# Kernel optimization log

Hardware: AMD Instinct MI355X
Metric: run time of the kernel (lower is better)

The kernel has to match this reference:

```python
import jax, jax.numpy as jnp
from jax import lax
import numpy as np

T = 8   # num_samples
D = 7   # num_nodes
K = 3   # topk


def _normalize(v):
    return v / jnp.maximum(jnp.linalg.norm(v, axis=-1, keepdims=True), 1e-12)


def _pool(x):
    # AdaptiveMaxPool2d(1): [B,H,N,C,h,w] -> [B,H,N,C]
    return x.max(axis=(-2, -1))


def _sepconv(x, dw, dwb, pw, pwb):
    # depthwise 3x3 (pad 1) + pointwise 1x1, NCHW
    c = x.shape[1]
    y = lax.conv_general_dilated(x, dw, (1, 1), ((1, 1), (1, 1)),
                                 dimension_numbers=('NCHW', 'OIHW', 'NCHW'),
                                 feature_group_count=c)
    y = y + dwb[None, :, None, None]
    y = lax.conv_general_dilated(y, pw, (1, 1), 'VALID',
                                 dimension_numbers=('NCHW', 'OIHW', 'NCHW'))
    return y + pwb[None, :, None, None]


def _conv_iter(x, A, dw, dwb, pw, pwb):
    # x: [B,H,N,C,h,w], A: [B,H,M,N] -> aggregate then sepconv update
    x = jnp.einsum('bhnm,bhmcij->bhncij', A, x)
    B, H, N, C, h, w = x.shape
    y = x.transpose(0, 2, 1, 3, 4, 5).reshape(B * N, H * C, h, w)
    y = _sepconv(y, dw, dwb, pw, pwb)
    return y.reshape(B, N, H, C, h, w).transpose(0, 2, 1, 3, 4, 5)


def reference(x, alpha_if, alpha_tm1, alpha_rev, alpha_tm2,
              bias_if, bias_tm1, bias_rev, bias_tm2,
              if_dw, if_dwb, if_pw, if_pwb,
              tm1_dw, tm1_dwb, tm1_pw, tm1_pwb,
              rev_dw, rev_dwb, rev_pw, rev_pwb,
              tm2_dw, tm2_dwb, tm2_pw, tm2_pwb,
              tr_dw, tr_dwb, tr_pw, tr_pwb):
    B, H, Nall, C, hh, ww = x.shape
    normal = x[:, :, 1:]            # [B,H,T*D,C,h,w]
    master = x[:, :, 0:1]           # [B,H,1,C,h,w]
    # 'b h (t d) c i j -> (b t) h d c i j'
    normal = normal.reshape(B, H, T, D, C, hh, ww).transpose(0, 2, 1, 3, 4, 5, 6).reshape(B * T, H, D, C, hh, ww)

    # inter-frame adjacency
    vn = _normalize(_pool(normal))
    A = jax.nn.softmax(jnp.einsum('bhnc,bhmc->bhnm', vn, vn) / alpha_if + bias_if, axis=-1)
    normal = _conv_iter(normal, A, if_dw, if_dwb, if_pw, if_pwb)

    # to master 1
    temp = normal.reshape(B, T, H, D, C, hh, ww).transpose(0, 2, 1, 3, 4, 5, 6).reshape(B, H, T * D, C, hh, ww)
    all_node = jnp.concatenate([master, temp], axis=2)   # [B,H,57,...]
    vn = _normalize(_pool(all_node))
    A = jax.nn.softmax(jnp.einsum('bhnc,bhmc->bhnm', vn[:, :, 0:1], vn) / alpha_tm1 + bias_tm1, axis=-1)
    master = _conv_iter(all_node, A, tm1_dw, tm1_dwb, tm1_pw, tm1_pwb)  # [B,H,1,C,h,w]

    # transform normal nodes
    Bt = B * T
    y = normal.transpose(0, 2, 1, 3, 4, 5).reshape(Bt * D, H * C, hh, ww)
    y = _sepconv(y, tr_dw, tr_dwb, tr_pw, tr_pwb)
    normal = y.reshape(Bt, D, H, C, hh, ww).transpose(0, 2, 1, 3, 4, 5)

    # reverse: topk MOST-DISSIMILAR frames (largest=False on similarity)
    temp = normal.reshape(B, T, H, D, C, hh, ww).transpose(0, 2, 1, 3, 4, 5, 6)  # [B,H,T,D,C,h,w]
    main = temp[:, :, :, -1]                                 # [B,H,T,C,h,w]
    mv = _normalize(_pool(main))                              # [B,H,T,C]
    Asim = jnp.einsum('bhtc,bhsc->bhts', mv, mv)
    idx = lax.top_k(-Asim, K)[1]                              # [B,H,T,K] smallest-sim frames
    bi = jnp.arange(B)[:, None, None, None]
    hi = jnp.arange(H)[None, :, None, None]
    sel = temp[bi, hi, idx]                                   # [B,H,T,K,D,C,h,w]
    different = sel.transpose(0, 2, 1, 3, 4, 5, 6, 7).reshape(Bt, H, K * D, C, hh, ww)

    vd = _normalize(_pool(different))
    vo = _normalize(_pool(normal))
    A = jax.nn.softmax(-jnp.einsum('bhnc,bhmc->bhnm', vo, vd) / alpha_rev + bias_rev, axis=-1)
    normal = _conv_iter(different, A, rev_dw, rev_dwb, rev_pw, rev_pwb) + normal

    # to master 2
    temp = normal.reshape(B, T, H, D, C, hh, ww).transpose(0, 2, 1, 3, 4, 5, 6).reshape(B, H, T * D, C, hh, ww)
    all_node = jnp.concatenate([master, temp], axis=2)
    vn = _normalize(_pool(all_node))
    A = jax.nn.softmax(jnp.einsum('bhnc,bhmc->bhnm', vn[:, :, 0:1], vn) / alpha_tm2 + bias_tm2, axis=-1)
    master = _conv_iter(all_node, A, tm2_dw, tm2_dwb, tm2_pw, tm2_pwb)
    return master[:, :, 0]                                    # [B,H,C,h,w]


def setup_inputs() -> dict:
    key = jax.random.key(0)
    ks = jax.random.split(key, 16)
    B, H, C, hh, ww = 4, 4, 128, 14, 14
    DIM = 512
    w_scale = 0.05

    def sep(k):
        k1, k2 = jax.random.split(k)
        return (jax.random.normal(k1, (DIM, 1, 3, 3), jnp.float32) * w_scale,
                jnp.zeros((DIM,), jnp.float32),
                jax.random.normal(k2, (DIM, DIM, 1, 1), jnp.float32) * w_scale,
                jnp.zeros((DIM,), jnp.float32))

    if_dw, if_dwb, if_pw, if_pwb = sep(ks[1])
    tm1_dw, tm1_dwb, tm1_pw, tm1_pwb = sep(ks[2])
    rev_dw, rev_dwb, rev_pw, rev_pwb = sep(ks[3])
    tm2_dw, tm2_dwb, tm2_pw, tm2_pwb = sep(ks[4])
    tr_dw, tr_dwb, tr_pw, tr_pwb = sep(ks[5])

    return dict(
        x=jax.random.normal(ks[0], (B, H, 1 + T * D, C, hh, ww), jnp.float32),
        alpha_if=jnp.ones((), jnp.float32), alpha_tm1=jnp.ones((), jnp.float32),
        alpha_rev=jnp.ones((), jnp.float32), alpha_tm2=jnp.ones((), jnp.float32),
        bias_if=jnp.zeros((D, D), jnp.float32),
        bias_tm1=jnp.zeros((1, 1 + T * D), jnp.float32),
        bias_rev=jnp.zeros((D, K * D), jnp.float32),
        bias_tm2=jnp.zeros((1, 1 + T * D), jnp.float32),
        if_dw=if_dw, if_dwb=if_dwb, if_pw=if_pw, if_pwb=if_pwb,
        tm1_dw=tm1_dw, tm1_dwb=tm1_dwb, tm1_pw=tm1_pw, tm1_pwb=tm1_pwb,
        rev_dw=rev_dw, rev_dwb=rev_dwb, rev_pw=rev_pw, rev_pwb=rev_pwb,
        tm2_dw=tm2_dw, tm2_dwb=tm2_dwb, tm2_pw=tm2_pw, tm2_pwb=tm2_pwb,
        tr_dw=tr_dw, tr_dwb=tr_dwb, tr_pw=tr_pw, tr_pwb=tr_pwb,
    )
```

## Files before the change

kernel.cpp:

```cpp
#include <hip/hip_runtime.h>
#include <hip/hip_bf16.h>
#include <float.h>
#include <math.h>

#define B_    4
#define H_    4
#define T_    8
#define D_    7
#define C_    128
#define HH_   14
#define S_    196
#define BT_   32
#define HC_   512
#define NODE_ 57
#define K_    3
#define KD_   21

#define BIG_  (BT_*D_*HC_*S_)
#define MS_   (B_*HC_*S_)
#define UB_   (BT_*D_*S_)
#define UM_   (B_*S_)
#define NT_   24
#define WS_   1024

typedef unsigned short u16;
typedef unsigned int   u32;
typedef short bf16x8 __attribute__((ext_vector_type(8)));
typedef float f32x4  __attribute__((ext_vector_type(4)));

__device__ __forceinline__ float wave_max(float v){
    #pragma unroll
    for(int o=32;o>0;o>>=1) v = fmaxf(v, __shfl_xor(v,o,64));
    return v;
}
__device__ __forceinline__ float wave_sum(float v){
    #pragma unroll
    for(int o=32;o>0;o>>=1) v += __shfl_xor(v,o,64);
    return v;
}
__device__ __forceinline__ u16 f2bf(float f){
    u32 u = __float_as_uint(f);
    u += 0x7FFF + ((u>>16)&1);
    return (u16)(u>>16);
}
__device__ __forceinline__ float bf2f(u16 h){ return __uint_as_float(((u32)h)<<16); }

__device__ __forceinline__ void gld16(const void* g, void* l){
    __builtin_amdgcn_global_load_lds(
        (__attribute__((address_space(1))) void*)(void*)g,
        (__attribute__((address_space(3))) void*)l, 16, 0, 0);
}

__global__ void k_pool_x(const float* __restrict__ x, float* __restrict__ out){
    int v = blockIdx.x*4 + (threadIdx.x>>6);
    int lane = threadIdx.x & 63;
    int c = v & (C_-1);
    int r = v >> 7;
    int d = r % D_; r /= D_;
    int h = r & (H_-1); r >>= 2;
    int bt = r;
    int b = bt >> 3, t = bt & 7;
    const float* row = x + ((size_t)((b*H_+h)*NODE_ + 1 + t*D_ + d)*C_ + c)*S_;
    float m = -FLT_MAX;
    for(int s=lane; s<S_; s+=64) m = fmaxf(m, row[s]);
    m = wave_max(m);
    if(lane==0) out[v] = m;
}

__global__ void k_pool_conv(const float* __restrict__ in, float* __restrict__ out){
    int v = blockIdx.x*4 + (threadIdx.x>>6);
    int lane = threadIdx.x & 63;
    int c = v & (C_-1);
    int r = v >> 7;
    int d = r % D_; r /= D_;
    int h = r & (H_-1); r >>= 2;
    int bt = r;
    const float* row = in + ((size_t)((bt*D_+d)*HC_ + h*C_ + c))*S_;
    float m = -FLT_MAX;
    for(int s=lane; s<S_; s+=64) m = fmaxf(m, row[s]);
    m = wave_max(m);
    if(lane==0) out[v] = m;
}

__global__ void k_pool_x_master(const float* __restrict__ x, float* __restrict__ out){
    int v = blockIdx.x*4 + (threadIdx.x>>6);
    int lane = threadIdx.x & 63;
    int c = v & (C_-1);
    int h = (v>>7) & (H_-1);
    int b = v >> 9;
    const float* row = x + ((size_t)((b*H_+h)*NODE_)*C_ + c)*S_;
    float m = -FLT_MAX;
    for(int s=lane; s<S_; s+=64) m = fmaxf(m, row[s]);
    m = wave_max(m);
    if(lane==0) out[v] = m;
}

__global__ void k_pool_m1(const float* __restrict__ in, float* __restrict__ out){
    int v = blockIdx.x*4 + (threadIdx.x>>6);
    int lane = threadIdx.x & 63;
    int c = v & (C_-1);
    int h = (v>>7) & (H_-1);
    int b = v >> 9;
    const float* row = in + ((size_t)(b*HC_ + h*C_ + c))*S_;
    float m = -FLT_MAX;
    for(int s=lane; s<S_; s+=64) m = fmaxf(m, row[s]);
    m = wave_max(m);
    if(lane==0) out[v] = m;
}

__global__ void k_normalize(float* __restrict__ v){
    int vec = blockIdx.x;
    float val = v[(size_t)vec*C_ + threadIdx.x];
    float ss = wave_sum(val*val);
    __shared__ float sh[2];
    if((threadIdx.x&63)==0) sh[threadIdx.x>>6] = ss;
    __syncthreads();
    float tot = sh[0]+sh[1];
    v[(size_t)vec*C_ + threadIdx.x] = val / fmaxf(sqrtf(tot), 1e-12f);
}

__global__ void k_A_if(const float* __restrict__ vn, const float* __restrict__ bias,
                       const float* __restrict__ alpha_p, float* __restrict__ A){
    int bh = blockIdx.x;
    __shared__ float vs[D_*C_];
    __shared__ float z[D_][D_];
    for(int e=threadIdx.x; e<D_*C_; e+=64) vs[e] = vn[(size_t)bh*D_*C_ + e];
    __syncthreads();
    float alpha = alpha_p[0];
    if(threadIdx.x < D_*D_){
        int n = threadIdx.x/D_, m = threadIdx.x%D_;
        float acc=0.f;
        for(int c=0;c<C_;c++) acc += vs[n*C_+c]*vs[m*C_+c];
        z[n][m] = acc/alpha + bias[n*D_+m];
    }
    __syncthreads();
    if(threadIdx.x < D_){
        int n = threadIdx.x;
        float mx=-FLT_MAX;
        for(int m=0;m<D_;m++) mx=fmaxf(mx,z[n][m]);
        float e[D_]; float sum=0.f;
        for(int m=0;m<D_;m++){ e[m]=expf(z[n][m]-mx); sum+=e[m]; }
        for(int m=0;m<D_;m++) A[((size_t)bh*D_+n)*D_+m] = e[m]/sum;
    }
}

__global__ void k_A_tm(const float* __restrict__ vm, const float* __restrict__ vnrm,
                       const float* __restrict__ bias, const float* __restrict__ alpha_p,
                       float* __restrict__ A){
    int bh = blockIdx.x;
    int b = bh>>2, h = bh&3;
    __shared__ float v0[C_];
    __shared__ float z[NODE_];
    for(int e=threadIdx.x;e<C_;e+=64) v0[e]=vm[(size_t)bh*C_+e];
    __syncthreads();
    float alpha=alpha_p[0];
    if(threadIdx.x<NODE_){
        int m=threadIdx.x;
        float acc=0.f;
        if(m==0){
            for(int c=0;c<C_;c++) acc+=v0[c]*v0[c];
        } else {
            int t=(m-1)/D_, d=(m-1)%D_;
            const float* vp = vnrm + (size_t)(((b*T_+t)*H_+h)*D_+d)*C_;
            for(int c=0;c<C_;c++) acc+=v0[c]*vp[c];
        }
        z[m]=acc/alpha + bias[m];
    }
    __syncthreads();
    if(threadIdx.x==0){
        float mx=-FLT_MAX;
        for(int m=0;m<NODE_;m++) mx=fmaxf(mx,z[m]);
        float sum=0.f;
        for(int m=0;m<NODE_;m++){ z[m]=expf(z[m]-mx); sum+=z[m]; }
        for(int m=0;m<NODE_;m++) A[(size_t)bh*NODE_+m]=z[m]/sum;
    }
}

__global__ void k_topk(const float* __restrict__ voHat, int* __restrict__ idx){
    int bh = blockIdx.x;
    int b = bh>>2, h = bh&3;
    __shared__ float mv[T_][C_];
    __shared__ float As[T_][T_];
    for(int e=threadIdx.x;e<T_*C_;e+=64){
        int t=e>>7, c=e&(C_-1);
        mv[t][c]=voHat[(size_t)(((b*T_+t)*H_+h)*D_+(D_-1))*C_+c];
    }
    __syncthreads();
    {
        int t=threadIdx.x>>3, s2=threadIdx.x&7;
        float acc=0.f;
        for(int c=0;c<C_;c++) acc+=mv[t][c]*mv[s2][c];
        As[t][s2]=acc;
    }
    __syncthreads();
    if(threadIdx.x<T_){
        int t=threadIdx.x;
        bool used[T_];
        for(int j=0;j<T_;j++) used[j]=false;
        for(int k=0;k<K_;k++){
            float mn=FLT_MAX; int bi=0;
            for(int s2=0;s2<T_;s2++){
                if(!used[s2] && As[t][s2]<mn){ mn=As[t][s2]; bi=s2; }
            }
            used[bi]=true;
            idx[((size_t)bh*T_+t)*K_+k]=bi;
        }
    }
}

__global__ void k_A_rev(const float* __restrict__ voHat, const int* __restrict__ idx,
                        const float* __restrict__ bias, const float* __restrict__ alpha_p,
                        float* __restrict__ A){
    int bth = blockIdx.x;
    int bt = bth>>2, h = bth&3;
    int b = bt>>3, t = bt&7;
    __shared__ float vo[D_][C_];
    __shared__ float vd[KD_][C_];
    __shared__ float z[D_][KD_];
    for(int e=threadIdx.x;e<D_*C_;e+=256){
        int n=e>>7, c=e&(C_-1);
        vo[n][c]=voHat[(size_t)((bt*H_+h)*D_+n)*C_+c];
    }
    for(int e=threadIdx.x;e<KD_*C_;e+=256){
        int m=e>>7, c=e&(C_-1);
        int k=m/D_, dp=m%D_;
        int tt=idx[((size_t)(b*H_+h)*T_+t)*K_+k];
        vd[m][c]=voHat[(size_t)(((b*T_+tt)*H_+h)*D_+dp)*C_+c];
    }
    __syncthreads();
    float alpha=alpha_p[0];
    if(threadIdx.x<D_*KD_){
        int n=threadIdx.x/KD_, m=threadIdx.x%KD_;
        float acc=0.f;
        for(int c=0;c<C_;c++) acc+=vo[n][c]*vd[m][c];
        z[n][m] = -acc/alpha + bias[n*KD_+m];
    }
    __syncthreads();
    if(threadIdx.x<D_){
        int n=threadIdx.x;
        float mx=-FLT_MAX;
        for(int m=0;m<KD_;m++) mx=fmaxf(mx,z[n][m]);
        float sum=0.f;
        for(int m=0;m<KD_;m++){ z[n][m]=expf(z[n][m]-mx); sum+=z[n][m]; }
        for(int m=0;m<KD_;m++) A[(size_t)((bt*H_+h)*D_+n)*KD_+m]=z[n][m]/sum;
    }
}

__launch_bounds__(256)
__global__ void k_agg_if(const float* __restrict__ x, const float* __restrict__ A,
                         float* __restrict__ out){
    int bt = blockIdx.x / 392;
    int p  = (blockIdx.x % 392)*256 + threadIdx.x;
    int b = bt>>3, t = bt&7;
    __shared__ float Ash[4][49];
    if(threadIdx.x < 196) Ash[threadIdx.x/49][threadIdx.x%49] = A[(size_t)bt*196 + threadIdx.x];
    __syncthreads();
    int hc = p / S_;
    int s  = p - hc*S_;
    int h = hc>>7, c = hc&127;
    const float* xp = x + ((size_t)((b*H_+h)*NODE_ + 1 + t*D_)*C_ + c)*S_ + s;
    float acc[D_];
    #pragma unroll
    for(int d=0;d<D_;d++) acc[d]=0.f;
    #pragma unroll
    for(int m=0;m<D_;m++){
        float xv = xp[(size_t)m*C_*S_];
        #pragma unroll
        for(int d=0;d<D_;d++) acc[d] += Ash[h][d*7+m]*xv;
    }
    size_t ob = ((size_t)bt*D_*HC_ + hc)*S_ + s;
    #pragma unroll
    for(int d=0;d<D_;d++) out[ob + (size_t)d*HC_*S_] = acc[d];
}

__launch_bounds__(256)
__global__ void k_agg_rev(const float* __restrict__ n2, const float* __restrict__ A,
                          const int* __restrict__ idx, float* __restrict__ out){
    int blk = blockIdx.x;
    int q  = blk % 98;
    int h  = (blk/98) & 3;
    int bt = blk / 392;
    int b = bt>>3, t = bt&7;
    int p  = q*256 + threadIdx.x;
    int c = p / S_;
    int s = p - c*S_;
    __shared__ float Ash[147];
    __shared__ int tts[3];
    if(threadIdx.x<147) Ash[threadIdx.x] = A[(size_t)(bt*4+h)*147 + threadIdx.x];
    if(threadIdx.x>=160 && threadIdx.x<163)
        tts[threadIdx.x-160] = idx[(size_t)((b*4+h)*8+t)*3 + (threadIdx.x-160)];
    __syncthreads();
    float acc[D_];
    #pragma unroll
    for(int d=0;d<D_;d++) acc[d]=0.f;
    #pragma unroll
    for(int k=0;k<K_;k++){
        int tt = tts[k];
        const float* np = n2 + ((size_t)((b*T_+tt)*D_)*HC_ + h*C_ + c)*S_ + s;
        #pragma unroll
        for(int dp=0;dp<D_;dp++){
            float xv = np[(size_t)dp*HC_*S_];
            #pragma unroll
            for(int d=0;d<D_;d++) acc[d] += Ash[d*21 + k*7 + dp]*xv;
        }
    }
    size_t ob = ((size_t)bt*D_*HC_ + h*C_ + c)*S_ + s;
    #pragma unroll
    for(int d=0;d<D_;d++) out[ob + (size_t)d*HC_*S_] = acc[d];
}

__global__ void k_agg_tm(const float* __restrict__ mastersrc, int master_is_x,
                         const float* __restrict__ normal, const float* __restrict__ A,
                         float* __restrict__ out){
    int i = blockIdx.x*256 + threadIdx.x;
    int s = i % S_;
    int r = i / S_;
    int hc = r & (HC_-1);
    int b = r >> 9;
    int h = hc >> 7, c = hc & (C_-1);
    const float* Ap = A + (size_t)(b*H_+h)*NODE_;
    float m0;
    if(master_is_x) m0 = mastersrc[((size_t)((b*H_+h)*NODE_)*C_ + c)*S_ + s];
    else            m0 = mastersrc[(size_t)(b*HC_+hc)*S_ + s];
    float acc = Ap[0]*m0;
    for(int t=0;t<T_;t++){
        const float* np = normal + ((size_t)((b*T_+t)*D_)*HC_+hc)*S_+s;
        #pragma unroll
        for(int d=0;d<D_;d++)
            acc += Ap[1+t*D_+d]*np[(size_t)d*HC_*S_];
    }
    out[i]=acc;
}

__launch_bounds__(256)
__global__ void k_dwsplit(const float* __restrict__ in, const float* __restrict__ w,
                          const float* __restrict__ bias,
                          u16* __restrict__ Xh, u16* __restrict__ Xl){
    int img = blockIdx.x >> 5;
    int ch0 = (blockIdx.x & 31) * 16;
    __shared__ float ti[16][S_];
    __shared__ float to[16][S_];
    int tid = threadIdx.x;
    for(int e=tid; e<16*S_; e+=256){
        int chl = e/S_, s = e%S_;
        ti[chl][s] = in[((size_t)img*HC_ + ch0 + chl)*S_ + s];
    }
    __syncthreads();
    for(int e=tid; e<16*S_; e+=256){
        int chl = e/S_, s = e%S_;
        int ch = ch0 + chl;
        int y = s/HH_, xx = s%HH_;
        float acc = bias[ch];
        #pragma unroll
        for(int ky=0;ky<3;ky++){
            int yy=y+ky-1;
            if(yy<0||yy>=HH_) continue;
            #pragma unroll
            for(int kx=0;kx<3;kx++){
                int xx2=xx+kx-1;
                if(xx2<0||xx2>=HH_) continue;
                acc += ti[chl][yy*HH_+xx2]*w[ch*9+ky*3+kx];
            }
        }
        to[chl][s]=acc;
    }
    __syncthreads();
    for(int e=tid; e<16*S_; e+=256){
        int s = e>>4, chl = e&15;
        float f = to[chl][s];
        u16 h = f2bf(f);
        float lo = f - bf2f(h);
        size_t o = ((size_t)img*S_ + s)*HC_ + ch0 + chl;
        Xh[o] = h;
        Xl[o] = f2bf(lo);
    }
}

__global__ void k_prepW(const float* __restrict__ Wg, u16* __restrict__ Waug){
    int i = blockIdx.x*256 + threadIdx.x;
    int oc = i >> 9, ic = i & 511;
    float f = Wg[i];
    u16 h = f2bf(f);
    float lo = f - bf2f(h);
    size_t base = (size_t)oc*WS_;
    Waug[base + ic]       = h;
    Waug[base + 512 + ic] = f2bf(lo);
}

__launch_bounds__(512)
__global__ void k_pwmfma(const u16* __restrict__ Xh, const u16* __restrict__ Xl,
                         const u16* __restrict__ Waug, const float* __restrict__ bias,
                         const float* __restrict__ res, float* __restrict__ out,
                         int nwg, int utot){
    __shared__ u16 SM[2][16384];
    const int tid  = threadIdx.x;
    const int q = nwg >> 3, r = nwg & 7;
    int xcd = blockIdx.x & 7, j = blockIdx.x >> 3;
    int L = xcd*q + (xcd < r ? xcd : r) + j;
    const int u0   = (L >> 2) * 128;
    const int oc0  = (L & 3) * 128;
    const int lane = tid & 63;
    const int w    = tid >> 6;
    const int wr   = w >> 1, wc = w & 1;
    const int l15  = lane & 15, lg = lane >> 4;

    f32x4 acc[2][4];
    #pragma unroll
    for(int mi=0;mi<2;mi++)
        #pragma unroll
        for(int ni=0;ni<4;ni++)
            acc[mi][ni] = (f32x4){0.f,0.f,0.f,0.f};

    auto STAGE = [&](int t){
        int jj, wk, xk; const u16* Xp;
        if(t < 16){ jj = t>>1; wk = (t&1) ? 512 + jj*64 : jj*64; Xp = Xh; xk = jj*64; }
        else      { jj = t-16; wk = jj*64;                        Xp = Xl; xk = jj*64; }
        u16* Asb = SM[t&1];
        u16* Bsb = Asb + 8192;
        #pragma unroll
        for(int i=0;i<2;i++){
            int seg = w*2 + i;
            int row = seg*8 + (lane>>3);
            int cg  = (lane&7) ^ (lane>>3);
            gld16(Waug + (size_t)(oc0+row)*WS_ + wk + cg*8, Asb + seg*512);
            gld16(Xp   + (size_t)(u0 +row)*512 + xk + cg*8, Bsb + seg*512);
        }
    };
    auto COMPUTE = [&](int cur){
        const u16* Asb = SM[cur];
        const u16* Bsb = SM[cur] + 8192;
        #pragma unroll
        for(int ks=0;ks<2;ks++){
            bf16x8 a[2], b[4];
            #pragma unroll
            for(int mi=0;mi<2;mi++){
                int row = wr*32 + mi*16 + l15;
                int ch  = ((ks<<2) + lg) ^ (row & 7);
                a[mi] = *(const bf16x8*)(Asb + row*64 + ch*8);
            }
            #pragma unroll
            for(int ni=0;ni<4;ni++){
                int row = wc*64 + ni*16 + l15;
                int ch  = ((ks<<2) + lg) ^ (row & 7);
                b[ni] = *(const bf16x8*)(Bsb + row*64 + ch*8);
            }
            #pragma unroll
            for(int mi=0;mi<2;mi++)
                #pragma unroll
                for(int ni=0;ni<4;ni++)
                    acc[mi][ni] = __builtin_amdgcn_mfma_f32_16x16x32_bf16(a[mi], b[ni], acc[mi][ni], 0,0,0);
        }
    };

    STAGE(0);
    for(int t=0; t<NT_; t++){
        if(t+1 < NT_){
            STAGE(t+1);
            asm volatile("s_waitcnt vmcnt(4)" ::: "memory");
        } else {
            asm volatile("s_waitcnt vmcnt(0)" ::: "memory");
        }
        __builtin_amdgcn_s_barrier();
        asm volatile("" ::: "memory");
        COMPUTE(t&1);
        asm volatile("" ::: "memory");
        __builtin_amdgcn_s_barrier();
    }

    #pragma unroll
    for(int ni=0;ni<4;ni++){
        int u = u0 + wc*64 + ni*16 + l15;
        if(u >= utot) continue;
        int img = u / S_, s = u - img*S_;
        #pragma unroll
        for(int mi=0;mi<2;mi++){
            int ocb = oc0 + wr*32 + mi*16 + lg*4;
            #pragma unroll
            for(int q2=0;q2<4;q2++){
                int oc = ocb + q2;
                size_t oidx = ((size_t)img*HC_ + oc)*S_ + s;
                float v = acc[mi][ni][q2] + bias[oc];
                if(res) v += res[oidx];
                out[oidx] = v;
            }
        }
    }
}

extern "C" void kernel_launch(void* const* d_in, const int* in_sizes, int n_in,
                              void* d_out, int out_size, void* d_ws, size_t ws_size,
                              hipStream_t stream){
    (void)in_sizes; (void)n_in; (void)out_size; (void)ws_size;
    const float* x         = (const float*)d_in[0];
    const float* alpha_if  = (const float*)d_in[1];
    const float* alpha_tm1 = (const float*)d_in[2];
    const float* alpha_rev = (const float*)d_in[3];
    const float* alpha_tm2 = (const float*)d_in[4];
    const float* bias_if   = (const float*)d_in[5];
    const float* bias_tm1  = (const float*)d_in[6];
    const float* bias_rev  = (const float*)d_in[7];
    const float* bias_tm2  = (const float*)d_in[8];
    const float* if_dw =(const float*)d_in[9];  const float* if_dwb =(const float*)d_in[10];
    const float* if_pw =(const float*)d_in[11]; const float* if_pwb =(const float*)d_in[12];
    const float* tm1_dw=(const float*)d_in[13]; const float* tm1_dwb=(const float*)d_in[14];
    const float* tm1_pw=(const float*)d_in[15]; const float* tm1_pwb=(const float*)d_in[16];
    const float* rev_dw=(const float*)d_in[17]; const float* rev_dwb=(const float*)d_in[18];
    const float* rev_pw=(const float*)d_in[19]; const float* rev_pwb=(const float*)d_in[20];
    const float* tm2_dw=(const float*)d_in[21]; const float* tm2_dwb=(const float*)d_in[22];
    const float* tm2_pw=(const float*)d_in[23]; const float* tm2_pwb=(const float*)d_in[24];
    const float* tr_dw =(const float*)d_in[25]; const float* tr_dwb =(const float*)d_in[26];
    const float* tr_pw =(const float*)d_in[27]; const float* tr_pwb =(const float*)d_in[28];

    float* ws = (float*)d_ws;
    float* G0      = ws;
    float* G1      = G0 + (size_t)BIG_;
    u16*   Xh      = (u16*)(ws + 2*(size_t)BIG_);
    u16*   Xl      = Xh + (size_t)BIG_;
    u16*   WA0     = Xl + (size_t)BIG_;
    u16*   WA1     = WA0 + 512*WS_;
    u16*   WA2     = WA1 + 512*WS_;
    u16*   WA3     = WA2 + 512*WS_;
    u16*   WA4     = WA3 + 512*WS_;
    float* master1 = (float*)(WA4 + 512*WS_);
    float* Ma      = master1 + MS_;
    float* pooledN = Ma + MS_;
    float* pooledM = pooledN + BT_*H_*D_*C_;
    float* Aif     = pooledM + B_*H_*C_;
    float* Atm1    = Aif + BT_*H_*D_*D_;
    float* Arev    = Atm1 + B_*H_*NODE_;
    float* Atm2    = Arev + BT_*H_*D_*KD_;
    int*   idxb    = (int*)(Atm2 + B_*H_*NODE_);
    float* out     = (float*)d_out;

    const int NV  = BT_*H_*D_*C_;
    const int gemmGrid  = (UB_/128)*4;
    const int gemmGridM = ((UM_+127)/128)*4;
    const int dsGrid  = BT_*D_*32;
    const int dsGridM = B_*32;
    const int aggGrid = BT_*392;

    k_prepW<<<1024, 256, 0, stream>>>(if_pw,  WA0);
    k_prepW<<<1024, 256, 0, stream>>>(tr_pw,  WA1);
    k_prepW<<<1024, 256, 0, stream>>>(rev_pw, WA2);
    k_prepW<<<1024, 256, 0, stream>>>(tm1_pw, WA3);
    k_prepW<<<1024, 256, 0, stream>>>(tm2_pw, WA4);

    k_pool_x   <<<NV/4, 256, 0, stream>>>(x, pooledN);
    k_normalize<<<NV/C_, 128, 0, stream>>>(pooledN);
    k_A_if     <<<BT_*H_, 64, 0, stream>>>(pooledN, bias_if, alpha_if, Aif);
    k_agg_if   <<<aggGrid, 256, 0, stream>>>(x, Aif, G0);
    k_dwsplit  <<<dsGrid, 256, 0, stream>>>(G0, if_dw, if_dwb, Xh, Xl);
    k_pwmfma   <<<gemmGrid, 512, 0, stream>>>(Xh, Xl, WA0, if_pwb, (const float*)nullptr, G1, gemmGrid, UB_);

    k_pool_conv<<<NV/4, 256, 0, stream>>>(G1, pooledN);
    k_normalize<<<NV/C_, 128, 0, stream>>>(pooledN);
    k_pool_x_master<<<(B_*H_*C_)/4, 256, 0, stream>>>(x, pooledM);
    k_normalize<<<B_*H_, 128, 0, stream>>>(pooledM);
    k_A_tm     <<<B_*H_, 64, 0, stream>>>(pooledM, pooledN, bias_tm1, alpha_tm1, Atm1);
    k_agg_tm   <<<MS_/256, 256, 0, stream>>>(x, 1, G1, Atm1, Ma);
    k_dwsplit  <<<dsGridM, 256, 0, stream>>>(Ma, tm1_dw, tm1_dwb, Xh, Xl);
    k_pwmfma   <<<gemmGridM, 512, 0, stream>>>(Xh, Xl, WA3, tm1_pwb, (const float*)nullptr, master1, gemmGridM, UM_);

    k_dwsplit  <<<dsGrid, 256, 0, stream>>>(G1, tr_dw, tr_dwb, Xh, Xl);
    k_pwmfma   <<<gemmGrid, 512, 0, stream>>>(Xh, Xl, WA1, tr_pwb, (const float*)nullptr, G0, gemmGrid, UB_);

    k_pool_conv<<<NV/4, 256, 0, stream>>>(G0, pooledN);
    k_normalize<<<NV/C_, 128, 0, stream>>>(pooledN);
    k_topk     <<<B_*H_, 64, 0, stream>>>(pooledN, idxb);
    k_A_rev    <<<BT_*H_, 256, 0, stream>>>(pooledN, idxb, bias_rev, alpha_rev, Arev);
    k_agg_rev  <<<aggGrid, 256, 0, stream>>>(G0, Arev, idxb, G1);
    k_dwsplit  <<<dsGrid, 256, 0, stream>>>(G1, rev_dw, rev_dwb, Xh, Xl);
    k_pwmfma   <<<gemmGrid, 512, 0, stream>>>(Xh, Xl, WA2, rev_pwb, G0, G1, gemmGrid, UB_);

    k_pool_conv<<<NV/4, 256, 0, stream>>>(G1, pooledN);
    k_normalize<<<NV/C_, 128, 0, stream>>>(pooledN);
    k_pool_m1  <<<(B_*H_*C_)/4, 256, 0, stream>>>(master1, pooledM);
    k_normalize<<<B_*H_, 128, 0, stream>>>(pooledM);
    k_A_tm     <<<B_*H_, 64, 0, stream>>>(pooledM, pooledN, bias_tm2, alpha_tm2, Atm2);
    k_agg_tm   <<<MS_/256, 256, 0, stream>>>(master1, 0, G1, Atm2, Ma);
    k_dwsplit  <<<dsGridM, 256, 0, stream>>>(Ma, tm2_dw, tm2_dwb, Xh, Xl);
    k_pwmfma   <<<gemmGridM, 512, 0, stream>>>(Xh, Xl, WA4, tm2_pwb, (const float*)nullptr, out, gemmGridM, UM_);
}
```

Before: 994.1 us.

## Fuse aggregation into depthwise conv and fold pooling into dwsplit

```diff
diff --git a/kernel.cpp b/kernel.cpp
--- a/kernel.cpp
+++ b/kernel.cpp
@@ -20,6 +20,7 @@
 #define MS_   (B_*HC_*S_)
 #define UB_   (BT_*D_*S_)
 #define UM_   (B_*S_)
+#define UMP_  896
 #define NT_   24
 #define WS_   1024
 
@@ -244,69 +245,6 @@
         for(int m=0;m<KD_;m++){ z[n][m]=expf(z[n][m]-mx); sum+=z[n][m]; }
         for(int m=0;m<KD_;m++) A[(size_t)((bt*H_+h)*D_+n)*KD_+m]=z[n][m]/sum;
     }
-}
-
-__launch_bounds__(256)
-__global__ void k_agg_if(const float* __restrict__ x, const float* __restrict__ A,
-                         float* __restrict__ out){
-    int bt = blockIdx.x / 392;
-    int p  = (blockIdx.x % 392)*256 + threadIdx.x;
-    int b = bt>>3, t = bt&7;
-    __shared__ float Ash[4][49];
-    if(threadIdx.x < 196) Ash[threadIdx.x/49][threadIdx.x%49] = A[(size_t)bt*196 + threadIdx.x];
-    __syncthreads();
-    int hc = p / S_;
-    int s  = p - hc*S_;
-    int h = hc>>7, c = hc&127;
-    const float* xp = x + ((size_t)((b*H_+h)*NODE_ + 1 + t*D_)*C_ + c)*S_ + s;
-    float acc[D_];
-    #pragma unroll
-    for(int d=0;d<D_;d++) acc[d]=0.f;
-    #pragma unroll
-    for(int m=0;m<D_;m++){
-        float xv = xp[(size_t)m*C_*S_];
-        #pragma unroll
-        for(int d=0;d<D_;d++) acc[d] += Ash[h][d*7+m]*xv;
-    }
-    size_t ob = ((size_t)bt*D_*HC_ + hc)*S_ + s;
-    #pragma unroll
-    for(int d=0;d<D_;d++) out[ob + (size_t)d*HC_*S_] = acc[d];
-}
-
-__launch_bounds__(256)
-__global__ void k_agg_rev(const float* __restrict__ n2, const float* __restrict__ A,
-                          const int* __restrict__ idx, float* __restrict__ out){
-    int blk = blockIdx.x;
-    int q  = blk % 98;
-    int h  = (blk/98) & 3;
-    int bt = blk / 392;
-    int b = bt>>3, t = bt&7;
-    int p  = q*256 + threadIdx.x;
-    int c = p / S_;
-    int s = p - c*S_;
-    __shared__ float Ash[147];
-    __shared__ int tts[3];
-    if(threadIdx.x<147) Ash[threadIdx.x] = A[(size_t)(bt*4+h)*147 + threadIdx.x];
-    if(threadIdx.x>=160 && threadIdx.x<163)
-        tts[threadIdx.x-160] = idx[(size_t)((b*4+h)*8+t)*3 + (threadIdx.x-160)];
-    __syncthreads();
-    float acc[D_];
-    #pragma unroll
-    for(int d=0;d<D_;d++) acc[d]=0.f;
-    #pragma unroll
-    for(int k=0;k<K_;k++){
-        int tt = tts[k];
-        const float* np = n2 + ((size_t)((b*T_+tt)*D_)*HC_ + h*C_ + c)*S_ + s;
-        #pragma unroll
-        for(int dp=0;dp<D_;dp++){
-            float xv = np[(size_t)dp*HC_*S_];
-            #pragma unroll
-            for(int d=0;d<D_;d++) acc[d] += Ash[d*21 + k*7 + dp]*xv;
-        }
-    }
-    size_t ob = ((size_t)bt*D_*HC_ + h*C_ + c)*S_ + s;
-    #pragma unroll
-    for(int d=0;d<D_;d++) out[ob + (size_t)d*HC_*S_] = acc[d];
 }
 
 __global__ void k_agg_tm(const float* __restrict__ mastersrc, int master_is_x,
@@ -332,6 +270,42 @@
     out[i]=acc;
 }
 
+__device__ __forceinline__ void dw_split_tail(float (*ti)[S_], float (*to)[S_],
+                                              const float* __restrict__ w,
+                                              const float* __restrict__ bias,
+                                              int img, int ch0,
+                                              u16* __restrict__ Xh, u16* __restrict__ Xl){
+    int tid = threadIdx.x;
+    for(int e=tid; e<16*S_; e+=256){
+        int chl = e/S_, s = e - (e/S_)*S_;
+        int ch = ch0 + chl;
+        int y = s/HH_, xx = s - (s/HH_)*HH_;
+        float acc = bias[ch];
+        #pragma unroll
+        for(int ky=0;ky<3;ky++){
+            int yy=y+ky-1;
+            if(yy<0||yy>=HH_) continue;
+            #pragma unroll
+            for(int kx=0;kx<3;kx++){
+                int xx2=xx+kx-1;
+                if(xx2<0||xx2>=HH_) continue;
+                acc += ti[chl][yy*HH_+xx2]*w[ch*9+ky*3+kx];
+            }
+        }
+        to[chl][s]=acc;
+    }
+    __syncthreads();
+    for(int e=tid; e<16*S_; e+=256){
+        int s = e>>4, chl = e&15;
+        float f = to[chl][s];
+        u16 h = f2bf(f);
+        float lo = f - bf2f(h);
+        size_t o = ((size_t)img*S_ + s)*HC_ + ch0 + chl;
+        Xh[o] = h;
+        Xl[o] = f2bf(lo);
+    }
+}
+
 __launch_bounds__(256)
 __global__ void k_dwsplit(const float* __restrict__ in, const float* __restrict__ w,
                           const float* __restrict__ bias,
@@ -342,38 +316,111 @@
     __shared__ float to[16][S_];
     int tid = threadIdx.x;
     for(int e=tid; e<16*S_; e+=256){
-        int chl = e/S_, s = e%S_;
+        int chl = e/S_, s = e - (e/S_)*S_;
         ti[chl][s] = in[((size_t)img*HC_ + ch0 + chl)*S_ + s];
     }
     __syncthreads();
+    dw_split_tail(ti, to, w, bias, img, ch0, Xh, Xl);
+}
+
+__launch_bounds__(256)
+__global__ void k_dwsplit_pool(const float* __restrict__ in, const float* __restrict__ w,
+                               const float* __restrict__ bias,
+                               u16* __restrict__ Xh, u16* __restrict__ Xl,
+                               float* __restrict__ pooled){
+    int img = blockIdx.x >> 5;
+    int ch0 = (blockIdx.x & 31) * 16;
+    __shared__ float ti[16][S_];
+    __shared__ float to[16][S_];
+    __shared__ float pm[16][17];
+    int tid = threadIdx.x;
     for(int e=tid; e<16*S_; e+=256){
-        int chl = e/S_, s = e%S_;
-        int ch = ch0 + chl;
-        int y = s/HH_, xx = s%HH_;
-        float acc = bias[ch];
-        #pragma unroll
-        for(int ky=0;ky<3;ky++){
-            int yy=y+ky-1;
-            if(yy<0||yy>=HH_) continue;
-            #pragma unroll
-            for(int kx=0;kx<3;kx++){
-                int xx2=xx+kx-1;
-                if(xx2<0||xx2>=HH_) continue;
-                acc += ti[chl][yy*HH_+xx2]*w[ch*9+ky*3+kx];
-            }
-        }
-        to[chl][s]=acc;
-    }
-    __syncthreads();
+        int chl = e/S_, s = e - (e/S_)*S_;
+        ti[chl][s] = in[((size_t)img*HC_ + ch0 + chl)*S_ + s];
+    }
+    __syncthreads();
+    dw_split_tail(ti, to, w, bias, img, ch0, Xh, Xl);
+    {
+        int chl = tid & 15, g = tid >> 4;
+        float m = -FLT_MAX;
+        for(int s=g; s<S_; s+=16) m = fmaxf(m, ti[chl][s]);
+        pm[chl][g] = m;
+    }
+    __syncthreads();
+    if(tid < 16){
+        float mm = -FLT_MAX;
+        #pragma unroll
+        for(int g2=0; g2<16; g2++) mm = fmaxf(mm, pm[tid][g2]);
+        int bt = img/7, d = img - (img/7)*7;
+        pooled[(size_t)((bt*4 + (ch0>>7))*7 + d)*C_ + (ch0 & 127) + tid] = mm;
+    }
+}
+
+__launch_bounds__(256)
+__global__ void k_fused_if(const float* __restrict__ x, const float* __restrict__ A,
+                           const float* __restrict__ w, const float* __restrict__ bias,
+                           u16* __restrict__ Xh, u16* __restrict__ Xl){
+    int img = blockIdx.x >> 5;
+    int ch0 = (blockIdx.x & 31) * 16;
+    int bt = img/7, d = img - bt*7;
+    int b = bt >> 3, t = bt & 7;
+    int h = ch0 >> 7, c0 = ch0 & 127;
+    __shared__ float ti[16][S_];
+    __shared__ float to[16][S_];
+    float a[D_];
+    #pragma unroll
+    for(int m=0;m<D_;m++) a[m] = A[(size_t)((bt*4+h)*D_ + d)*D_ + m];
+    int tid = threadIdx.x;
+    const float* xb = x + ((size_t)((b*H_+h)*NODE_ + 1 + t*D_)*C_ + c0)*S_;
     for(int e=tid; e<16*S_; e+=256){
-        int s = e>>4, chl = e&15;
-        float f = to[chl][s];
-        u16 h = f2bf(f);
-        float lo = f - bf2f(h);
-        size_t o = ((size_t)img*S_ + s)*HC_ + ch0 + chl;
-        Xh[o] = h;
-        Xl[o] = f2bf(lo);
-    }
+        int chl = e/S_, s = e - (e/S_)*S_;
+        const float* xp = xb + (size_t)chl*S_ + s;
+        float acc = 0.f;
+        #pragma unroll
+        for(int m=0;m<D_;m++) acc += a[m]*xp[(size_t)m*C_*S_];
+        ti[chl][s] = acc;
+    }
+    __syncthreads();
+    dw_split_tail(ti, to, w, bias, img, ch0, Xh, Xl);
+}
+
+__launch_bounds__(256)
+__global__ void k_fused_rev(const float* __restrict__ n2, const float* __restrict__ A,
+                            const int* __restrict__ idx,
+                            const float* __restrict__ w, const float* __restrict__ bias,
+                            u16* __restrict__ Xh, u16* __restrict__ Xl){
+    int img = blockIdx.x >> 5;
+    int ch0 = (blockIdx.x & 31) * 16;
+    int bt = img/7, d = img - bt*7;
+    int b = bt >> 3, t = bt & 7;
+    int h = ch0 >> 7;
+    __shared__ float ti[16][S_];
+    __shared__ float to[16][S_];
+    float a[KD_];
+    #pragma unroll
+    for(int j=0;j<KD_;j++) a[j] = A[(size_t)((bt*4+h)*D_ + d)*KD_ + j];
+    int tt0 = idx[((size_t)(b*H_+h)*T_+t)*K_+0];
+    int tt1 = idx[((size_t)(b*H_+h)*T_+t)*K_+1];
+    int tt2 = idx[((size_t)(b*H_+h)*T_+t)*K_+2];
+    const float* p0 = n2 + ((size_t)((b*T_+tt0)*D_)*HC_ + ch0)*S_;
+    const float* p1 = n2 + ((size_t)((b*T_+tt1)*D_)*HC_ + ch0)*S_;
+    const float* p2 = n2 + ((size_t)((b*T_+tt2)*D_)*HC_ + ch0)*S_;
+    int tid = threadIdx.x;
+    for(int e=tid; e<16*S_; e+=256){
+        int chl = e/S_, s = e - (e/S_)*S_;
+        size_t off = (size_t)chl*S_ + s;
+        float acc = 0.f;
+        #pragma unroll
+        for(int dp=0;dp<D_;dp++){
+            size_t o2 = off + (size_t)dp*HC_*S_;
+            acc += a[dp]      * p0[o2];
+            acc += a[D_+dp]   * p1[o2];
+            acc += a[2*D_+dp] * p2[o2];
+        }
+        ti[chl][s] = acc;
+    }
+    __syncthreads();
+    dw_split_tail(ti, to, w, bias, img, ch0, Xh, Xl);
 }
 
 __global__ void k_prepW(const float* __restrict__ Wg, u16* __restrict__ Waug){
@@ -521,7 +568,9 @@
     u16*   WA2     = WA1 + 512*WS_;
     u16*   WA3     = WA2 + 512*WS_;
     u16*   WA4     = WA3 + 512*WS_;
-    float* master1 = (float*)(WA4 + 512*WS_);
+    u16*   XhM     = WA4 + 512*WS_;
+    u16*   XlM     = XhM + (size_t)UMP_*HC_;
+    float* master1 = (float*)(XlM + (size_t)UMP_*HC_);
     float* Ma      = master1 + MS_;
     float* pooledN = Ma + MS_;
     float* pooledM = pooledN + BT_*H_*D_*C_;
@@ -534,10 +583,10 @@
 
     const int NV  = BT_*H_*D_*C_;
     const int gemmGrid  = (UB_/128)*4;
-    const int gemmGridM = ((UM_+127)/128)*4;
+    const int gemmGridM = (UMP_/128)*4;
     const int dsGrid  = BT_*D_*32;
     const int dsGridM = B_*32;
-    const int aggGrid = BT_*392;
+    float* null_res = nullptr;
 
     k_prepW<<<1024, 256, 0, stream>>>(if_pw,  WA0);
     k_prepW<<<1024, 256, 0, stream>>>(tr_pw,  WA1);
@@ -548,28 +597,24 @@
     k_pool_x   <<<NV/4, 256, 0, stream>>>(x, pooledN);
     k_normalize<<<NV/C_, 128, 0, stream>>>(pooledN);
     k_A_if     <<<BT_*H_, 64, 0, stream>>>(pooledN, bias_if, alpha_if, Aif);
-    k_agg_if   <<<aggGrid, 256, 0, stream>>>(x, Aif, G0);
-    k_dwsplit  <<<dsGrid, 256, 0, stream>>>(G0, if_dw, if_dwb, Xh, Xl);
-    k_pwmfma   <<<gemmGrid, 512, 0, stream>>>(Xh, Xl, WA0, if_pwb, (const float*)nullptr, G1, gemmGrid, UB_);
-
-    k_pool_conv<<<NV/4, 256, 0, stream>>>(G1, pooledN);
+    k_fused_if <<<dsGrid, 256, 0, stream>>>(x, Aif, if_dw, if_dwb, Xh, Xl);
+    k_pwmfma   <<<gemmGrid, 512, 0, stream>>>(Xh, Xl, WA0, if_pwb, null_res, G1, gemmGrid, UB_);
+
+    k_dwsplit_pool<<<dsGrid, 256, 0, stream>>>(G1, tr_dw, tr_dwb, Xh, Xl, pooledN);
     k_normalize<<<NV/C_, 128, 0, stream>>>(pooledN);
     k_pool_x_master<<<(B_*H_*C_)/4, 256, 0, stream>>>(x, pooledM);
     k_normalize<<<B_*H_, 128, 0, stream>>>(pooledM);
     k_A_tm     <<<B_*H_, 64, 0, stream>>>(pooledM, pooledN, bias_tm1, alpha_tm1, Atm1);
     k_agg_tm   <<<MS_/256, 256, 0, stream>>>(x, 1, G1, Atm1, Ma);
-    k_dwsplit  <<<dsGridM, 256, 0, stream>>>(Ma, tm1_dw, tm1_dwb, Xh, Xl);
-    k_pwmfma   <<<gemmGridM, 512, 0, stream>>>(Xh, Xl, WA3, tm1_pwb, (const float*)nullptr, master1, gemmGridM, UM_);
-
-    k_dwsplit  <<<dsGrid, 256, 0, stream>>>(G1, tr_dw, tr_dwb, Xh, Xl);
-    k_pwmfma   <<<gemmGrid, 512, 0, stream>>>(Xh, Xl, WA1, tr_pwb, (const float*)nullptr, G0, gemmGrid, UB_);
+    k_dwsplit  <<<dsGridM, 256, 0, stream>>>(Ma, tm1_dw, tm1_dwb, XhM, XlM);
+    k_pwmfma   <<<gemmGridM, 512, 0, stream>>>(XhM, XlM, WA3, tm1_pwb, null_res, master1, gemmGridM, UM_);
+    k_pwmfma   <<<gemmGrid, 512, 0, stream>>>(Xh, Xl, WA1, tr_pwb, null_res, G0, gemmGrid, UB_);
 
     k_pool_conv<<<NV/4, 256, 0, stream>>>(G0, pooledN);
     k_normalize<<<NV/C_, 128, 0, stream>>>(pooledN);
     k_topk     <<<B_*H_, 64, 0, stream>>>(pooledN, idxb);
     k_A_rev    <<<BT_*H_, 256, 0, stream>>>(pooledN, idxb, bias_rev, alpha_rev, Arev);
-    k_agg_rev  <<<aggGrid, 256, 0, stream>>>(G0, Arev, idxb, G1);
-    k_dwsplit  <<<dsGrid, 256, 0, stream>>>(G1, rev_dw, rev_dwb, Xh, Xl);
+    k_fused_rev<<<dsGrid, 256, 0, stream>>>(G0, Arev, idxb, rev_dw, rev_dwb, Xh, Xl);
     k_pwmfma   <<<gemmGrid, 512, 0, stream>>>(Xh, Xl, WA2, rev_pwb, G0, G1, gemmGrid, UB_);
 
     k_pool_conv<<<NV/4, 256, 0, stream>>>(G1, pooledN);
@@ -578,6 +623,6 @@
     k_normalize<<<B_*H_, 128, 0, stream>>>(pooledM);
     k_A_tm     <<<B_*H_, 64, 0, stream>>>(pooledM, pooledN, bias_tm2, alpha_tm2, Atm2);
     k_agg_tm   <<<MS_/256, 256, 0, stream>>>(master1, 0, G1, Atm2, Ma);
-    k_dwsplit  <<<dsGridM, 256, 0, stream>>>(Ma, tm2_dw, tm2_dwb, Xh, Xl);
-    k_pwmfma   <<<gemmGridM, 512, 0, stream>>>(Xh, Xl, WA4, tm2_pwb, (const float*)nullptr, out, gemmGridM, UM_);
-}
+    k_dwsplit  <<<dsGridM, 256, 0, stream>>>(Ma, tm2_dw, tm2_dwb, XhM, XlM);
+    k_pwmfma   <<<gemmGridM, 512, 0, stream>>>(XhM, XlM, WA4, tm2_pwb, null_res, out, gemmGridM, UM_);
+}
```

New measurement: 977.9 us. About the same (-1.6%).
